# Performance work log

Measured on AMD Instinct MI355X. Metric: run time of the kernel, lower is better.

## Reference

```python
import jax, jax.numpy as jnp
import numpy as np

D = 1024
NH = 16
HD = D // NH  # 64

def setup_inputs() -> dict:
    key = jax.random.key(0)
    ks = jax.random.split(key, 6)
    s = 1.0 / np.sqrt(D)
    x = jax.random.normal(ks[0], (4, 2048, D), dtype=jnp.float32)
    Wq = jax.random.normal(ks[1], (D, D), dtype=jnp.float32) * s
    Wk = jax.random.normal(ks[2], (D, D), dtype=jnp.float32) * s
    Wv = jax.random.normal(ks[3], (D, D), dtype=jnp.float32) * s
    Wo = jax.random.normal(ks[4], (D, D), dtype=jnp.float32) * s
    bo = jnp.zeros((D,), dtype=jnp.float32)
    return {"x": x, "Wq": Wq, "Wk": Wk, "Wv": Wv, "Wo": Wo, "bo": bo}

def reference(x, Wq, Wk, Wv, Wo, bo):
    B, N, _ = x.shape
    # conv1d(kernel=1, no bias) == linear with weight [out, in]
    q = jnp.einsum('bnd,ed->bne', x, Wq).reshape(B, N, NH, HD)
    k = jnp.einsum('bnd,ed->bne', x, Wk).reshape(B, N, NH, HD)
    v = jnp.einsum('bnd,ed->bne', x, Wv).reshape(B, N, NH, HD)
    scores = jnp.einsum('bqhd,bkhd->bhqk', q, k) / jnp.sqrt(jnp.float32(HD))
    attn = jax.nn.softmax(scores, axis=-1)
    out = jnp.einsum('bhqk,bkhd->bqhd', attn, v).reshape(B, N, D)
    # out_proj: Linear(D, D)
    out = jnp.einsum('bnd,ed->bne', out, Wo) + bo
    return out
```

## Files before the change

### kernel.cpp

```cpp
#include <hip/hip_runtime.h>
#include <stdint.h>

typedef unsigned short u16;
typedef __attribute__((__ext_vector_type__(4))) float f32x4;
typedef __attribute__((__ext_vector_type__(8))) __bf16 bf16x8;
typedef __attribute__((__ext_vector_type__(4))) unsigned short u16x4;
typedef __attribute__((__ext_vector_type__(8))) unsigned short u16x8;

#define DEV static __device__ __forceinline__

DEV u16 f2b(float f) {
  union { float f; unsigned u; } v; v.f = f;
  unsigned r = v.u + 0x7FFFu + ((v.u >> 16) & 1u);
  return (u16)(r >> 16);
}

typedef const __attribute__((address_space(1))) void* gas_t;
typedef __attribute__((address_space(3))) void* las_t;

DEV void gl_lds16(const void* g, void* l) {
  __builtin_amdgcn_global_load_lds((gas_t)(uintptr_t)g, (las_t)(uint32_t)(uintptr_t)l,
                                   16, 0, 0);
}

__global__ void cvt4(const float* __restrict__ s, u16* __restrict__ d, int n4) {
  const int i = blockIdx.x * 256 + threadIdx.x;
  if (i >= n4) return;
  const float4 f = reinterpret_cast<const float4*>(s)[i];
  u16x4 o;
  o.x = f2b(f.x); o.y = f2b(f.y); o.z = f2b(f.z); o.w = f2b(f.w);
  reinterpret_cast<u16x4*>(d)[i] = o;
}

__global__ void cvtW(const float* __restrict__ Wq, const float* __restrict__ Wk,
                     const float* __restrict__ Wv, const float* __restrict__ Wo,
                     u16* __restrict__ Wqkv, u16* __restrict__ Wob) {
  const int bid = blockIdx.x, sel = bid >> 10;
  const int i = (bid & 1023) * 256 + threadIdx.x;
  const float* s = sel == 0 ? Wq : sel == 1 ? Wk : sel == 2 ? Wv : Wo;
  u16* d = (sel == 3) ? Wob : Wqkv + sel * 1048576;
  const float4 f = reinterpret_cast<const float4*>(s)[i];
  u16x4 o;
  o.x = f2b(f.x); o.y = f2b(f.y); o.z = f2b(f.z); o.w = f2b(f.w);
  reinterpret_cast<u16x4*>(d)[i] = o;
}

template<int MODE>
__global__ __launch_bounds__(256, 2) void gemm_bt(
    const u16* __restrict__ A, const u16* __restrict__ B, int K, int tiles_n,
    u16* __restrict__ Qo, u16* __restrict__ Ko, u16* __restrict__ Vo,
    float* __restrict__ Fo, const float* __restrict__ bias, int N)
{
  __shared__ u16 smem[32768];
  const int nwg = gridDim.x;
  const int bid = blockIdx.x;
  const int swz = (bid & 7) * (nwg >> 3) + (bid >> 3);
  const int tm = swz / tiles_n, tn = swz % tiles_n;
  const int tid = threadIdx.x, wid = tid >> 6, lane = tid & 63;
  const int wr = wid >> 1, wc = wid & 1;
  const int lr = lane & 15, lk = lane >> 4;

  const f32x4 fz = {0.f, 0.f, 0.f, 0.f};
  f32x4 acc[4][4];
#pragma unroll
  for (int i = 0; i < 4; i++)
#pragma unroll
    for (int j = 0; j < 4; j++) acc[i][j] = fz;

  const u16* Ab = A + (size_t)tm * 128 * K;
  const u16* Bb = B + (size_t)tn * 128 * K;

  auto stage = [&](int kt, int buf) {
    u16* As = smem + buf * 16384;
    u16* Bs = As + 8192;
#pragma unroll
    for (int i = 0; i < 4; i++) {
      const int c = tid + 256 * i;
      const int r = c >> 3;
      const int col = kt * 64 + (((c & 7) ^ (r & 7)) * 8);
      gl_lds16(Ab + (size_t)r * K + col, &As[(i * 256 + wid * 64) * 8]);
      gl_lds16(Bb + (size_t)r * K + col, &Bs[(i * 256 + wid * 64) * 8]);
    }
  };

  const int nt = K >> 6;
  stage(0, 0);
  for (int t = 0; t < nt; t++) {
    const int cur = t & 1;
    asm volatile("s_waitcnt vmcnt(0)" ::: "memory");
    asm volatile("s_barrier" ::: "memory");
    if (t + 1 < nt) stage(t + 1, cur ^ 1);
    const u16* As = smem + cur * 16384;
    const u16* Bs = As + 8192;
#pragma unroll
    for (int kk = 0; kk < 2; kk++) {
      bf16x8 af[4], bf[4];
#pragma unroll
      for (int i = 0; i < 4; i++) {
        const int row = wr * 64 + i * 16 + lr;
        af[i] = *reinterpret_cast<const bf16x8*>(
            &As[row * 64 + (((kk * 4 + lk) ^ (row & 7)) * 8)]);
      }
#pragma unroll
      for (int j = 0; j < 4; j++) {
        const int row = wc * 64 + j * 16 + lr;
        bf[j] = *reinterpret_cast<const bf16x8*>(
            &Bs[row * 64 + (((kk * 4 + lk) ^ (row & 7)) * 8)]);
      }
#pragma unroll
      for (int i = 0; i < 4; i++)
#pragma unroll
        for (int j = 0; j < 4; j++)
          acc[i][j] = __builtin_amdgcn_mfma_f32_16x16x32_bf16(af[i], bf[j], acc[i][j], 0, 0, 0);
    }
  }

  const int row0 = tm * 128 + wr * 64;
  if constexpr (MODE == 0) {
    const int mat = (tn * 128) >> 10;
    if (mat < 2) {
      u16* Mo = (mat == 0) ? Qo : Ko;
      const float qs = (mat == 0) ? 0.18033688f : 1.0f;
#pragma unroll
      for (int i = 0; i < 4; i++) {
#pragma unroll
        for (int j = 0; j < 4; j++) {
          const int e0 = tn * 128 + wc * 64 + j * 16;
          const int h = (e0 & 1023) >> 6;
          const int d = (e0 & 63) + lr;
#pragma unroll
          for (int r = 0; r < 4; r++) {
            const int m = row0 + i * 16 + lk * 4 + r;
            const int bb = m >> 11, n = m & 2047;
            Mo[((bb * 16 + h) * 2048 + n) * 64 + d] = f2b(acc[i][j][r] * qs);
          }
        }
      }
    } else {
      __syncthreads();
#pragma unroll
      for (int i = 0; i < 4; i++) {
#pragma unroll
        for (int j = 0; j < 4; j++) {
          const int e = wc * 64 + j * 16 + lr;
          const int m4 = wr * 64 + i * 16 + lk * 4;
          u16x4 pk;
#pragma unroll
          for (int r = 0; r < 4; r++) pk[r] = f2b(acc[i][j][r]);
          *reinterpret_cast<u16x4*>(&smem[e * 128 + (m4 ^ ((e & 7) << 3))]) = pk;
        }
      }
      __syncthreads();
      const int e = tid >> 1, half = tid & 1;
      const int ch = tn * 128 + e;
      const int hh = (ch >> 6) & 15, d = ch & 63;
      const int bb = (tm * 128) >> 11, n0 = (tm * 128) & 2047;
      u16* Vrow = Vo + ((size_t)((bb * 16 + hh) * 64 + d)) * 2048 + n0 + half * 64;
      const int xe = (e & 7) << 3;
#pragma unroll
      for (int s = 0; s < 8; s++) {
        const int npl = half * 64 + s * 8;
        const int nA = (npl & ~31) | ((npl >> 1) & 12);
        const u16x4 a = *reinterpret_cast<const u16x4*>(&smem[e * 128 + (nA ^ xe)]);
        const u16x4 b = *reinterpret_cast<const u16x4*>(&smem[e * 128 + ((nA + 16) ^ xe)]);
        u16x8 o;
#pragma unroll
        for (int r = 0; r < 4; r++) { o[r] = a[r]; o[4 + r] = b[r]; }
        *reinterpret_cast<u16x8*>(&Vrow[s * 8]) = o;
      }
    }
  } else {
#pragma unroll
    for (int i = 0; i < 4; i++) {
#pragma unroll
      for (int j = 0; j < 4; j++) {
        const int col = tn * 128 + wc * 64 + j * 16 + lr;
        const float bv = bias[col];
#pragma unroll
        for (int r = 0; r < 4; r++) {
          const int m = row0 + i * 16 + lk * 4 + r;
          Fo[(size_t)m * N + col] = acc[i][j][r] + bv;
        }
      }
    }
  }
}

__global__ __launch_bounds__(512, 2) void attn_fwd(
    const u16* __restrict__ Q, const u16* __restrict__ K, const u16* __restrict__ Vt,
    u16* __restrict__ O)
{
  __shared__ u16 Ks[2][64 * 64];
  __shared__ u16 Vs[2][64 * 64];
  const int bh = blockIdx.x >> 3, qt = blockIdx.x & 7;
  const int tid = threadIdx.x, w = tid >> 6, lane = tid & 63;
  const int lr = lane & 15, lk = lane >> 4;
  const u16* Qp = Q + ((size_t)bh * 2048 + qt * 256) * 64;
  const u16* Kp = K + (size_t)bh * 2048 * 64;
  const u16* Vp = Vt + (size_t)bh * 64 * 2048;

  bf16x8 qfr[2][2];
#pragma unroll
  for (int qf = 0; qf < 2; qf++)
#pragma unroll
    for (int kk = 0; kk < 2; kk++)
      qfr[qf][kk] = *reinterpret_cast<const bf16x8*>(
          &Qp[(w * 32 + qf * 16 + lr) * 64 + kk * 32 + lk * 8]);

  bf16x8 onesf;
#pragma unroll
  for (int j = 0; j < 8; j++) onesf[j] = (__bf16)1.0f;

  const f32x4 fz = {0.f, 0.f, 0.f, 0.f};
  f32x4 oacc[2][4];
  f32x4 lacc[2] = {fz, fz};
#pragma unroll
  for (int qf = 0; qf < 2; qf++)
#pragma unroll
    for (int df = 0; df < 4; df++) oacc[qf][df] = fz;

  auto stage = [&](int kt, int buf) {
    const int c = tid;
    const int r = c >> 3, ss = ((c & 7) ^ (r & 7)) * 8;
    gl_lds16(Kp + (size_t)(kt * 64 + r) * 64 + ss, &Ks[buf][w * 512]);
    gl_lds16(Vp + (size_t)r * 2048 + kt * 64 + ss, &Vs[buf][w * 512]);
  };

  stage(0, 0);
  for (int kt = 0; kt < 32; kt++) {
    const int cur = kt & 1;
    asm volatile("s_waitcnt vmcnt(0)" ::: "memory");
    __syncthreads();
    if (kt < 31) stage(kt + 1, cur ^ 1);

    f32x4 sacc[2][4];
#pragma unroll
    for (int kf = 0; kf < 4; kf++) {
      const int row = kf * 16 + lr;
      const bf16x8 kfr = *reinterpret_cast<const bf16x8*>(
          &Ks[cur][row * 64 + ((lk ^ (row & 7)) * 8)]);
      sacc[0][kf] = __builtin_amdgcn_mfma_f32_16x16x32_bf16(kfr, qfr[0][0], fz, 0, 0, 0);
      sacc[1][kf] = __builtin_amdgcn_mfma_f32_16x16x32_bf16(kfr, qfr[1][0], fz, 0, 0, 0);
    }
#pragma unroll
    for (int kf = 0; kf < 4; kf++) {
      const int row = kf * 16 + lr;
      const bf16x8 kfr = *reinterpret_cast<const bf16x8*>(
          &Ks[cur][row * 64 + (((4 + lk) ^ (row & 7)) * 8)]);
      sacc[0][kf] = __builtin_amdgcn_mfma_f32_16x16x32_bf16(kfr, qfr[0][1], sacc[0][kf], 0, 0, 0);
      sacc[1][kf] = __builtin_amdgcn_mfma_f32_16x16x32_bf16(kfr, qfr[1][1], sacc[1][kf], 0, 0, 0);
    }

    bf16x8 pa[2][2];
#pragma unroll
    for (int qf = 0; qf < 2; qf++) {
#pragma unroll
      for (int kf = 0; kf < 4; kf++)
#pragma unroll
        for (int r = 0; r < 4; r++)
          sacc[qf][kf][r] = __builtin_amdgcn_exp2f(sacc[qf][kf][r]);
#pragma unroll
      for (int kk = 0; kk < 2; kk++)
#pragma unroll
        for (int j = 0; j < 4; j++) {
          pa[qf][kk][j]     = (__bf16)sacc[qf][2 * kk][j];
          pa[qf][kk][4 + j] = (__bf16)sacc[qf][2 * kk + 1][j];
        }
      lacc[qf] = __builtin_amdgcn_mfma_f32_16x16x32_bf16(pa[qf][0], onesf, lacc[qf], 0, 0, 0);
      lacc[qf] = __builtin_amdgcn_mfma_f32_16x16x32_bf16(pa[qf][1], onesf, lacc[qf], 0, 0, 0);
    }

#pragma unroll
    for (int df = 0; df < 4; df++) {
      const int d = df * 16 + lr;
#pragma unroll
      for (int kk = 0; kk < 2; kk++) {
        bf16x8 vfr = *reinterpret_cast<const bf16x8*>(
            &Vs[cur][d * 64 + (((kk * 4 + lk) ^ (d & 7)) * 8)]);
        oacc[0][df] = __builtin_amdgcn_mfma_f32_16x16x32_bf16(pa[0][kk], vfr, oacc[0][df], 0, 0, 0);
        oacc[1][df] = __builtin_amdgcn_mfma_f32_16x16x32_bf16(pa[1][kk], vfr, oacc[1][df], 0, 0, 0);
      }
    }
  }

  const int b = bh >> 4, h = bh & 15;
#pragma unroll
  for (int qf = 0; qf < 2; qf++) {
    float iv[4];
#pragma unroll
    for (int r = 0; r < 4; r++) iv[r] = 1.f / lacc[qf][r];
#pragma unroll
    for (int df = 0; df < 4; df++)
#pragma unroll
      for (int r = 0; r < 4; r++) {
        const int n = qt * 256 + w * 32 + qf * 16 + lk * 4 + r;
        O[((size_t)b * 2048 + n) * 1024 + h * 64 + df * 16 + lr] =
            f2b(oacc[qf][df][r] * iv[r]);
      }
  }
}

extern "C" void kernel_launch(void* const* d_in, const int* in_sizes, int n_in,
                              void* d_out, int out_size, void* d_ws, size_t ws_size,
                              hipStream_t stream) {
  const float* x  = (const float*)d_in[0];
  const float* Wq = (const float*)d_in[1];
  const float* Wk = (const float*)d_in[2];
  const float* Wv = (const float*)d_in[3];
  const float* Wo = (const float*)d_in[4];
  const float* bo = (const float*)d_in[5];
  float* out = (float*)d_out;

  u16* ws   = (u16*)d_ws;
  u16* xb   = ws;
  u16* Wqkv = xb + 8388608;
  u16* Wob  = Wqkv + 3145728;
  u16* Qb   = Wob + 1048576;
  u16* Kb   = Qb + 8388608;
  u16* Vtb  = Kb + 8388608;

  cvt4<<<8192, 256, 0, stream>>>(x, xb, 2097152);
  cvtW<<<4096, 256, 0, stream>>>(Wq, Wk, Wv, Wo, Wqkv, Wob);

  gemm_bt<0><<<64 * 24, 256, 0, stream>>>(xb, Wqkv, 1024, 24,
                                          Qb, Kb, Vtb, nullptr, nullptr, 3072);
  attn_fwd<<<512, 512, 0, stream>>>(Qb, Kb, Vtb, xb);
  gemm_bt<1><<<64 * 8, 256, 0, stream>>>(xb, Wob, 1024, 8,
                                         nullptr, nullptr, nullptr, out, bo, 1024);
}
```

Baseline: 161.5 us.

## Use 256x128 tiles with 8 waves and triple-buffered GEMM pipeline

The projection GEMMs move from 128x128 tiles with 4 waves and double buffering to 256x128 tiles with 8 waves and a three-stage LDS ring. Loads for stage t+2 are split across the two k-substeps and issued between fragment reads and MFMAs, with partial vmcnt waits and s_setprio around the MFMA block. The goals are more reuse of each B tile, more load latency hidden behind compute, and MFMA issue priority. In exchange it uses much more shared memory, so only one block fits per CU, adds extra barriers per k-step, and halves the grid size.

Measured after the change: 167.4 us. 1.04x slower.

```diff
diff --git a/kernel.cpp b/kernel.cpp
--- a/kernel.cpp
+++ b/kernel.cpp
@@ -46,18 +46,18 @@
 }
 
 template<int MODE>
-__global__ __launch_bounds__(256, 2) void gemm_bt(
+__global__ __launch_bounds__(512, 1) void gemm8p(
     const u16* __restrict__ A, const u16* __restrict__ B, int K, int tiles_n,
     u16* __restrict__ Qo, u16* __restrict__ Ko, u16* __restrict__ Vo,
     float* __restrict__ Fo, const float* __restrict__ bias, int N)
 {
-  __shared__ u16 smem[32768];
+  __shared__ u16 smem[73728];
   const int nwg = gridDim.x;
   const int bid = blockIdx.x;
   const int swz = (bid & 7) * (nwg >> 3) + (bid >> 3);
   const int tm = swz / tiles_n, tn = swz % tiles_n;
   const int tid = threadIdx.x, wid = tid >> 6, lane = tid & 63;
-  const int wr = wid >> 1, wc = wid & 1;
+  const int wm = wid >> 1, wn = wid & 1;
   const int lr = lane & 15, lk = lane >> 4;
 
   const f32x4 fz = {0.f, 0.f, 0.f, 0.f};
@@ -67,55 +67,65 @@
 #pragma unroll
     for (int j = 0; j < 4; j++) acc[i][j] = fz;
 
-  const u16* Ab = A + (size_t)tm * 128 * K;
+  const u16* Ab = A + (size_t)tm * 256 * K;
   const u16* Bb = B + (size_t)tn * 128 * K;
 
-  auto stage = [&](int kt, int buf) {
-    u16* As = smem + buf * 16384;
-    u16* Bs = As + 8192;
-#pragma unroll
-    for (int i = 0; i < 4; i++) {
-      const int c = tid + 256 * i;
+  auto stage = [&](int kt, int buf, int part) {
+    u16* As = smem + buf * 24576;
+    u16* Bs = As + 16384;
+#pragma unroll
+    for (int i = 0; i < 2; i++) {
+      const int c = tid + 512 * (part * 2 + i);
       const int r = c >> 3;
       const int col = kt * 64 + (((c & 7) ^ (r & 7)) * 8);
-      gl_lds16(Ab + (size_t)r * K + col, &As[(i * 256 + wid * 64) * 8]);
-      gl_lds16(Bb + (size_t)r * K + col, &Bs[(i * 256 + wid * 64) * 8]);
+      gl_lds16(Ab + (size_t)r * K + col, &As[((part * 2 + i) * 512 + wid * 64) * 8]);
+    }
+    {
+      const int c = tid + 512 * part;
+      const int r = c >> 3;
+      const int col = kt * 64 + (((c & 7) ^ (r & 7)) * 8);
+      gl_lds16(Bb + (size_t)r * K + col, &Bs[(part * 512 + wid * 64) * 8]);
     }
   };
 
   const int nt = K >> 6;
-  stage(0, 0);
+  stage(0, 0, 0); stage(0, 0, 1);
+  stage(1, 1, 0); stage(1, 1, 1);
   for (int t = 0; t < nt; t++) {
-    const int cur = t & 1;
-    asm volatile("s_waitcnt vmcnt(0)" ::: "memory");
+    const int cur = t % 3;
+    if (t < nt - 2) asm volatile("s_waitcnt vmcnt(6)" ::: "memory");
+    else            asm volatile("s_waitcnt vmcnt(0)" ::: "memory");
     asm volatile("s_barrier" ::: "memory");
-    if (t + 1 < nt) stage(t + 1, cur ^ 1);
-    const u16* As = smem + cur * 16384;
-    const u16* Bs = As + 8192;
+    const u16* As = smem + cur * 24576;
+    const u16* Bs = As + 16384;
 #pragma unroll
     for (int kk = 0; kk < 2; kk++) {
       bf16x8 af[4], bf[4];
 #pragma unroll
       for (int i = 0; i < 4; i++) {
-        const int row = wr * 64 + i * 16 + lr;
+        const int row = wm * 64 + i * 16 + lr;
         af[i] = *reinterpret_cast<const bf16x8*>(
             &As[row * 64 + (((kk * 4 + lk) ^ (row & 7)) * 8)]);
       }
 #pragma unroll
       for (int j = 0; j < 4; j++) {
-        const int row = wc * 64 + j * 16 + lr;
+        const int row = wn * 64 + j * 16 + lr;
         bf[j] = *reinterpret_cast<const bf16x8*>(
             &Bs[row * 64 + (((kk * 4 + lk) ^ (row & 7)) * 8)]);
       }
+      if (t + 2 < nt) stage(t + 2, (t + 2) % 3, kk);
+      asm volatile("s_barrier" ::: "memory");
+      __builtin_amdgcn_s_setprio(1);
 #pragma unroll
       for (int i = 0; i < 4; i++)
 #pragma unroll
         for (int j = 0; j < 4; j++)
           acc[i][j] = __builtin_amdgcn_mfma_f32_16x16x32_bf16(af[i], bf[j], acc[i][j], 0, 0, 0);
+      __builtin_amdgcn_s_setprio(0);
+      asm volatile("s_barrier" ::: "memory");
     }
   }
 
-  const int row0 = tm * 128 + wr * 64;
   if constexpr (MODE == 0) {
     const int mat = (tn * 128) >> 10;
     if (mat < 2) {
@@ -125,12 +135,12 @@
       for (int i = 0; i < 4; i++) {
 #pragma unroll
         for (int j = 0; j < 4; j++) {
-          const int e0 = tn * 128 + wc * 64 + j * 16;
+          const int e0 = tn * 128 + wn * 64 + j * 16;
           const int h = (e0 & 1023) >> 6;
           const int d = (e0 & 63) + lr;
 #pragma unroll
           for (int r = 0; r < 4; r++) {
-            const int m = row0 + i * 16 + lk * 4 + r;
+            const int m = tm * 256 + wm * 64 + i * 16 + lk * 4 + r;
             const int bb = m >> 11, n = m & 2047;
             Mo[((bb * 16 + h) * 2048 + n) * 64 + d] = f2b(acc[i][j][r] * qs);
           }
@@ -142,31 +152,31 @@
       for (int i = 0; i < 4; i++) {
 #pragma unroll
         for (int j = 0; j < 4; j++) {
-          const int e = wc * 64 + j * 16 + lr;
-          const int m4 = wr * 64 + i * 16 + lk * 4;
+          const int e = wn * 64 + j * 16 + lr;
+          const int m4 = wm * 64 + i * 16 + lk * 4;
           u16x4 pk;
 #pragma unroll
           for (int r = 0; r < 4; r++) pk[r] = f2b(acc[i][j][r]);
-          *reinterpret_cast<u16x4*>(&smem[e * 128 + (m4 ^ ((e & 7) << 3))]) = pk;
+          *reinterpret_cast<u16x4*>(&smem[e * 256 + (m4 ^ ((e & 7) << 3))]) = pk;
         }
       }
       __syncthreads();
-      const int e = tid >> 1, half = tid & 1;
-      const int ch = tn * 128 + e;
-      const int hh = (ch >> 6) & 15, d = ch & 63;
-      const int bb = (tm * 128) >> 11, n0 = (tm * 128) & 2047;
-      u16* Vrow = Vo + ((size_t)((bb * 16 + hh) * 64 + d)) * 2048 + n0 + half * 64;
+      const int e = tid >> 2, quarter = tid & 3;
+      const int ch = (tn - 16) * 128 + e;
+      const int hh = ch >> 6, d = ch & 63;
+      const int bb = tm >> 3, n0 = (tm * 256) & 2047;
+      u16* Vrow = Vo + ((size_t)((bb * 16 + hh) * 64 + d)) * 2048 + n0;
       const int xe = (e & 7) << 3;
 #pragma unroll
       for (int s = 0; s < 8; s++) {
-        const int npl = half * 64 + s * 8;
+        const int npl = quarter * 64 + s * 8;
         const int nA = (npl & ~31) | ((npl >> 1) & 12);
-        const u16x4 a = *reinterpret_cast<const u16x4*>(&smem[e * 128 + (nA ^ xe)]);
-        const u16x4 b = *reinterpret_cast<const u16x4*>(&smem[e * 128 + ((nA + 16) ^ xe)]);
+        const u16x4 a = *reinterpret_cast<const u16x4*>(&smem[e * 256 + (nA ^ xe)]);
+        const u16x4 b = *reinterpret_cast<const u16x4*>(&smem[e * 256 + ((nA + 16) ^ xe)]);
         u16x8 o;
 #pragma unroll
         for (int r = 0; r < 4; r++) { o[r] = a[r]; o[4 + r] = b[r]; }
-        *reinterpret_cast<u16x8*>(&Vrow[s * 8]) = o;
+        *reinterpret_cast<u16x8*>(&Vrow[npl]) = o;
       }
     }
   } else {
@@ -174,11 +184,11 @@
     for (int i = 0; i < 4; i++) {
 #pragma unroll
       for (int j = 0; j < 4; j++) {
-        const int col = tn * 128 + wc * 64 + j * 16 + lr;
+        const int col = tn * 128 + wn * 64 + j * 16 + lr;
         const float bv = bias[col];
 #pragma unroll
         for (int r = 0; r < 4; r++) {
-          const int m = row0 + i * 16 + lk * 4 + r;
+          const int m = tm * 256 + wm * 64 + i * 16 + lk * 4 + r;
           Fo[(size_t)m * N + col] = acc[i][j][r] + bv;
         }
       }
@@ -322,9 +332,9 @@
   cvt4<<<8192, 256, 0, stream>>>(x, xb, 2097152);
   cvtW<<<4096, 256, 0, stream>>>(Wq, Wk, Wv, Wo, Wqkv, Wob);
 
-  gemm_bt<0><<<64 * 24, 256, 0, stream>>>(xb, Wqkv, 1024, 24,
-                                          Qb, Kb, Vtb, nullptr, nullptr, 3072);
+  gemm8p<0><<<768, 512, 0, stream>>>(xb, Wqkv, 1024, 24,
+                                     Qb, Kb, Vtb, nullptr, nullptr, 3072);
   attn_fwd<<<512, 512, 0, stream>>>(Qb, Kb, Vtb, xb);
-  gemm_bt<1><<<64 * 8, 256, 0, stream>>>(xb, Wob, 1024, 8,
-                                         nullptr, nullptr, nullptr, out, bo, 1024);
-}
+  gemm8p<1><<<256, 512, 0, stream>>>(xb, Wob, 1024, 8,
+                                     nullptr, nullptr, nullptr, out, bo, 1024);
+}
```
